# Optimization experiments

Measured on AMD Instinct MI355X. Metric: run time of the kernel, lower is better.

## Reference

```python
import jax, jax.numpy as jnp
import numpy as np

N_NODES = 10000
N_EDGES = 320000
F_NODE = 16
NUM_BESSEL = 8
M = 32           # env_embed_multiplicity
LAT = 128        # latent dimension
R_MAX = 5.0
P_CUT = 6.0      # polynomial cutoff order
AVG_NEIGH = 32.0
SQRT3 = 1.7320508075688772
SQRT2 = 1.4142135623730951


def _mlp(x, weights):
    # nequip ScalarMLPFunction: linear layers with 1/sqrt(fan_in) norm, silu between layers
    h = x
    n = len(weights)
    for i, W in enumerate(weights):
        h = h @ W * (1.0 / np.sqrt(W.shape[0]))
        if i < n - 1:
            h = jax.nn.silu(h)
    return h


def _weight_channels(Y, w):
    # MakeWeightedChannels: Y [E,4] = (0e | 1e), w [E,M,2] per-irrep weights -> [E,M,4]
    return jnp.concatenate([w[..., 0:1] * Y[:, None, 0:1],
                            w[..., 1:2] * Y[:, None, 1:4]], axis=-1)


def setup_inputs():
    key = jax.random.key(0)
    ks = jax.random.split(key, 16)

    def w(k, i, o):
        return jax.random.normal(k, (i, o), jnp.float32)

    two_body_in = 2 * F_NODE + NUM_BESSEL  # 40
    return {
        "coordinates": jax.random.uniform(ks[0], (N_NODES, 3), jnp.float32),
        "node_attrs": jax.random.uniform(ks[1], (N_NODES, F_NODE), jnp.float32),
        "edge_index": jax.random.randint(ks[2], (2, N_EDGES), 0, N_NODES),
        "W2b0": w(ks[3], two_body_in, 64),
        "W2b1": w(ks[4], 64, 128),
        "W2b2": w(ks[5], 128, LAT),
        "Wenv0": w(ks[6], LAT, 4 * M),       # initial-edge embed + env weights (2 irreps each)
        "Wlat0": w(ks[7], LAT + 2 * M, 128),
        "Wlat1": w(ks[8], 128, LAT),
        "Ws0": w(ks[9], 2 * M, M),            # e3nn Linear, scalar block (2 paths)
        "Wv0": w(ks[10], 3 * M, M),           # e3nn Linear, vector block (3 paths)
        "Wenv1": w(ks[11], LAT, 2 * M),
        "Wfin0": w(ks[12], LAT + 2 * M, 128),
        "Wfin1": w(ks[13], 128, LAT),
    }


def reference(coordinates, node_attrs, edge_index, W2b0, W2b1, W2b2, Wenv0,
              Wlat0, Wlat1, Ws0, Wv0, Wenv1, Wfin0, Wfin1):
    sender, center = edge_index[0], edge_index[1]
    vec = coordinates[center] - coordinates[sender]            # [E,3]
    r = jnp.sqrt(jnp.sum(vec * vec, axis=-1) + 1e-12)          # [E]
    u = r / R_MAX
    p = P_CUT
    fcut = (1.0 - (p + 1.0) * (p + 2.0) / 2.0 * u**p
            + p * (p + 2.0) * u**(p + 1.0)
            - p * (p + 1.0) / 2.0 * u**(p + 2.0))
    fcut = jnp.where(u < 1.0, fcut, 0.0)
    n = jnp.arange(1, NUM_BESSEL + 1, dtype=jnp.float32)
    bessel = np.sqrt(2.0 / R_MAX) * jnp.sin(n * jnp.pi * u[:, None]) / r[:, None]
    edge_feats = bessel * fcut[:, None]                        # [E,8]
    unit = vec / r[:, None]
    Y = jnp.concatenate([jnp.ones_like(r)[:, None], SQRT3 * unit], axis=-1)  # [E,4] component-normalized SH

    inv_sqrt_n = 1.0 / np.sqrt(AVG_NEIGH)
    E = r.shape[0]

    # two-body latent (layer 0)
    lat_in = jnp.concatenate([node_attrs[center], node_attrs[sender], edge_feats], -1)
    lat = _mlp(lat_in, (W2b0, W2b1, W2b2)) * fcut[:, None]     # [E,LAT]
    w_all = lat @ Wenv0 * (1.0 / np.sqrt(LAT))                 # [E,4M]
    w_edge = w_all[:, :2 * M].reshape(E, M, 2)
    w_env = w_all[:, 2 * M:].reshape(E, M, 2)
    feat = _weight_channels(Y, w_edge)                         # [E,M,4] initial edge embed
    env = jax.ops.segment_sum(_weight_channels(Y, w_env), center, num_segments=N_NODES)
    env = env[center] * inv_sqrt_n                             # [E,M,4]

    fs, fv = feat[..., 0], feat[..., 1:]
    es, ev = env[..., 0], env[..., 1:]
    # layer-0 tensor product instruction list (uuu, no weights)
    p0 = fs * es                               # 0e x 0e -> 0e
    p1 = jnp.sum(fv * ev, -1) / SQRT3          # 1e x 1e -> 0e
    p2 = fs[..., None] * ev                    # 0e x 1e -> 1e
    p3 = fv * es[..., None]                    # 1e x 0e -> 1e
    p4 = jnp.cross(fv, ev) / SQRT2             # 1e x 1e -> 1e
    scal0 = jnp.concatenate([p0, p1], -1)      # [E,2M] scalar outs (n_scalar_outs=2)
    # per-layer e3nn Linear
    s_mix = scal0 @ Ws0 * (1.0 / np.sqrt(2 * M))                         # [E,M]
    v_mix = jnp.einsum('eic,io->eoc', jnp.concatenate([p2, p3, p4], 1), Wv0) * (1.0 / np.sqrt(3 * M))  # [E,M,3]

    # latent resnet update (update param 0 -> sigmoid = 0.5)
    alpha = 0.5
    c_old = 1.0 / np.sqrt(alpha * alpha + 1.0)
    c_new = alpha * c_old
    new_lat = _mlp(jnp.concatenate([lat, scal0], -1), (Wlat0, Wlat1)) * fcut[:, None]
    lat = c_old * lat + c_new * new_lat

    # layer 1 env embedding + tensor product (last layer -> scalars only)
    w_env1 = (lat @ Wenv1 * (1.0 / np.sqrt(LAT))).reshape(E, M, 2)
    env1 = jax.ops.segment_sum(_weight_channels(Y, w_env1), center, num_segments=N_NODES)
    env1 = env1[center] * inv_sqrt_n
    q0 = s_mix * env1[..., 0]
    q1 = jnp.sum(v_mix * env1[..., 1:], -1) / SQRT3
    scal1 = jnp.concatenate([q0, q1], -1)      # [E,2M]

    new_lat = _mlp(jnp.concatenate([lat, scal1], -1), (Wfin0, Wfin1)) * fcut[:, None]
    lat = c_old * lat + c_new * new_lat

    node_out = jax.ops.segment_sum(lat, center, num_segments=N_NODES) * inv_sqrt_n
    return node_out
```

## Files before the change

kernel.cpp:

```cpp
#include <hip/hip_runtime.h>
#include <hip/hip_bf16.h>
#include <math.h>

typedef __hip_bfloat16 bf16;
typedef unsigned short us;
typedef __attribute__((ext_vector_type(8))) short short8;
typedef __attribute__((ext_vector_type(4))) float floatx4;

#define AMODE_PLAIN  0
#define AMODE_CONCAT 2
#define EPI_SPLIT    1
#define EPI_STORE    2
#define EPI_FCUT     3
#define EPI_RESID    4

#define INV_SQRT_N 0.17677669529663687f
#define INV_SQRT3  0.5773502691896258f
#define INV_SQRT2  0.7071067811865476f
#define C_OLD      0.8944271909999159f
#define C_NEW      0.4472135954999579f
#define PI_F       3.14159265358979323846f
#define SQRT3_F    1.7320508075688772f
#define BESSEL_PREF 0.6324555320336759f

__device__ __forceinline__ float b2f(bf16 x) { return __bfloat162float(x); }
__device__ __forceinline__ bf16  f2b(float x) { return __float2bfloat16(x); }
__device__ __forceinline__ us f2bu(float x) {
  bf16 h = f2b(x); us u; __builtin_memcpy(&u, &h, 2); return u;
}
__device__ __forceinline__ float silu_f(float v) { return v / (1.f + __expf(-v)); }
__device__ __forceinline__ floatx4 mfma16(short8 a, short8 b, floatx4 c) {
  return __builtin_amdgcn_mfma_f32_16x16x32_bf16(a, b, c, 0, 0, 0);
}
__device__ __forceinline__ short8 ld8(const void* p) {
  return *reinterpret_cast<const short8*>(p);
}

__global__ __launch_bounds__(256) void k_deg(
    const int* __restrict__ eidx, int E, int* __restrict__ deg) {
  int e = blockIdx.x * 256 + threadIdx.x;
  if (e < E) atomicAdd(&deg[eidx[E + e]], 1);
}

__global__ __launch_bounds__(1024) void k_scan(
    const int* __restrict__ deg, int N,
    int* __restrict__ rowptr, int* __restrict__ cursor) {
  __shared__ int part[1024];
  int t = threadIdx.x;
  int C = (N + 1023) / 1024;
  int base = t * C;
  int s = 0;
  for (int i = 0; i < C; ++i) { int idx = base + i; if (idx < N) s += deg[idx]; }
  part[t] = s;
  __syncthreads();
  for (int off = 1; off < 1024; off <<= 1) {
    int v = (t >= off) ? part[t - off] : 0;
    __syncthreads();
    part[t] += v;
    __syncthreads();
  }
  int excl = (t == 0) ? 0 : part[t - 1];
  for (int i = 0; i < C; ++i) {
    int idx = base + i;
    if (idx < N) { rowptr[idx] = excl; cursor[idx] = excl; excl += deg[idx]; }
  }
  if (t == 0) rowptr[N] = part[1023];
}

__global__ __launch_bounds__(256) void k_fill(
    const int* __restrict__ eidx, int E, int* __restrict__ cursor,
    int* __restrict__ eord, int* __restrict__ cent) {
  int e = blockIdx.x * 256 + threadIdx.x;
  if (e >= E) return;
  int c = eidx[E + e];
  int slot = atomicAdd(&cursor[c], 1);
  eord[slot] = e;
  cent[slot] = c;
}

__global__ __launch_bounds__(256) void k_geom(
    const float* __restrict__ coords, const float* __restrict__ nattr,
    const int* __restrict__ eidx, const int* __restrict__ eord, int E,
    float* __restrict__ fcut, float* __restrict__ Yb, bf16* __restrict__ a64) {
  int j = blockIdx.x * 256 + threadIdx.x;
  if (j >= E) return;
  int e = eord[j];
  int s = eidx[e], c = eidx[E + e];
  float dx = coords[c*3+0] - coords[s*3+0];
  float dy = coords[c*3+1] - coords[s*3+1];
  float dz = coords[c*3+2] - coords[s*3+2];
  float r = sqrtf(dx*dx + dy*dy + dz*dz + 1e-12f);
  float u = r * 0.2f;
  float u3 = u*u*u;
  float u6 = u3*u3, u7 = u6*u, u8 = u7*u;
  float fc = 1.f - 28.f*u6 + 48.f*u7 - 21.f*u8;
  fc = (u < 1.f) ? fc : 0.f;
  float inv_r = 1.f / r;
  fcut[j] = fc;
  Yb[j*4+0] = 1.f;
  Yb[j*4+1] = SQRT3_F * dx * inv_r;
  Yb[j*4+2] = SQRT3_F * dy * inv_r;
  Yb[j*4+3] = SQRT3_F * dz * inv_r;
  bf16* row = a64 + (long)j * 64;
  #pragma unroll
  for (int i = 0; i < 16; ++i) row[i]      = f2b(nattr[(long)c*16 + i]);
  #pragma unroll
  for (int i = 0; i < 16; ++i) row[16 + i] = f2b(nattr[(long)s*16 + i]);
  float pref = BESSEL_PREF * inv_r * fc;
  #pragma unroll
  for (int n = 1; n <= 8; ++n)
    row[32 + n - 1] = f2b(pref * sinf((float)n * PI_F * u));
  #pragma unroll
  for (int i = 40; i < 64; ++i) row[i] = f2b(0.f);
}

__device__ __forceinline__ void wp(const float* W, us* Wt, int K, int NOUT, int t) {
  int n = t / K, k = t % K;
  Wt[n * K + k] = f2bu(W[k * NOUT + n]);
}

__global__ __launch_bounds__(256) void k_wprep_all(
    const float* W2b0, const float* W2b1, const float* W2b2,
    const float* Wenv0, const float* Wlat0, const float* Wlat1,
    const float* Wenv1, const float* Wfin0, const float* Wfin1,
    const float* Ws0, const float* Wv0,
    us* W2b0p, us* W2b1t, us* W2b2t, us* Wenv0t, us* Wlat0t, us* Wlat1t,
    us* Wenv1t, us* Wfin0t, us* Wfin1t, us* Wmixt) {
  int t = blockIdx.x * 256 + threadIdx.x;
  if (t < 8192)  { wp(W2b1,  W2b1t,  64, 128, t); return; } t -= 8192;
  if (t < 16384) { wp(W2b2,  W2b2t, 128, 128, t); return; } t -= 16384;
  if (t < 16384) { wp(Wenv0, Wenv0t,128, 128, t); return; } t -= 16384;
  if (t < 24576) { wp(Wlat0, Wlat0t,192, 128, t); return; } t -= 24576;
  if (t < 16384) { wp(Wlat1, Wlat1t,128, 128, t); return; } t -= 16384;
  if (t < 8192)  { wp(Wenv1, Wenv1t,128,  64, t); return; } t -= 8192;
  if (t < 24576) { wp(Wfin0, Wfin0t,192, 128, t); return; } t -= 24576;
  if (t < 16384) { wp(Wfin1, Wfin1t,128, 128, t); return; } t -= 16384;
  if (t < 4096)  {
    int n = t >> 6, k = t & 63;
    W2b0p[n * 64 + k] = (k < 40) ? f2bu(W2b0[k * 64 + n]) : 0;
    return;
  } t -= 4096;
  if (t < 5120) {
    int o = t / 160, k = t % 160;
    float v = (k < 64) ? Ws0[k * 32 + o] : Wv0[(k - 64) * 32 + o];
    Wmixt[o * 160 + k] = f2bu(v);
  }
}

__global__ __launch_bounds__(256) void k_envg(
    const bf16* __restrict__ wenv, const float* __restrict__ Yb,
    const int* __restrict__ rowptr, int N, float* __restrict__ env) {
  int t = blockIdx.x * 256 + threadIdx.x;
  if (t >= N * 32) return;
  int n = t >> 5, m = t & 31;
  int j0 = rowptr[n], j1 = rowptr[n + 1];
  float a0 = 0.f, a1 = 0.f, a2 = 0.f, a3 = 0.f;
  for (int j = j0; j < j1; ++j) {
    float w0 = b2f(wenv[(long)j*64 + 2*m]);
    float w1 = b2f(wenv[(long)j*64 + 2*m + 1]);
    float4 y = *reinterpret_cast<const float4*>(&Yb[(long)j*4]);
    a0 += w0;
    a1 += w1 * y.y;
    a2 += w1 * y.z;
    a3 += w1 * y.w;
  }
  *reinterpret_cast<float4*>(&env[(long)n*128 + m*4]) = make_float4(a0, a1, a2, a3);
}

__global__ __launch_bounds__(256) void k_nodeg(
    const bf16* __restrict__ lat, const int* __restrict__ rowptr,
    int N, float* __restrict__ out) {
  int t = blockIdx.x * 256 + threadIdx.x;
  if (t >= N * 128) return;
  int n = t >> 7, j = t & 127;
  int j0 = rowptr[n], j1 = rowptr[n + 1];
  float s = 0.f;
  for (int q = j0; q < j1; ++q)
    s += b2f(lat[(long)q*128 + j]);
  out[t] = s * INV_SQRT_N;
}

template<int K, int NOUT, int EPI>
__global__ __launch_bounds__(256) void mgemm(
    const bf16* __restrict__ A, const us* __restrict__ Wt,
    bf16* __restrict__ out1, bf16* __restrict__ out2, float scale, int E) {
  constexpr int CT = NOUT / 64;
  int tid = threadIdx.x;
  int lane = tid & 63, w = tid >> 6;
  int nl = lane & 15, quad = lane >> 4;
  long e0 = (long)blockIdx.x * 64;

  floatx4 acc[4][CT];
  #pragma unroll
  for (int i = 0; i < 4; ++i)
    #pragma unroll
    for (int j = 0; j < CT; ++j) acc[i][j] = (floatx4){0.f,0.f,0.f,0.f};

  for (int k0 = 0; k0 < K; k0 += 32) {
    int kk = k0 + quad * 8;
    short8 af[4], bv[CT];
    #pragma unroll
    for (int et = 0; et < 4; ++et) {
      long eg = e0 + et*16 + nl;
      af[et] = (eg < E) ? ld8(A + eg * (long)K + kk) : (short8){0,0,0,0,0,0,0,0};
    }
    #pragma unroll
    for (int ct = 0; ct < CT; ++ct)
      bv[ct] = ld8(Wt + (long)(w*CT*16 + ct*16 + nl) * K + kk);
    #pragma unroll
    for (int et = 0; et < 4; ++et)
      #pragma unroll
      for (int ct = 0; ct < CT; ++ct)
        acc[et][ct] = mfma16(af[et], bv[ct], acc[et][ct]);
  }

  #pragma unroll
  for (int et = 0; et < 4; ++et)
    #pragma unroll
    for (int ct = 0; ct < CT; ++ct)
      #pragma unroll
      for (int r = 0; r < 4; ++r) {
        long eg = e0 + et*16 + quad*4 + r;
        if (eg >= E) continue;
        int col = w*CT*16 + ct*16 + nl;
        float v = acc[et][ct][r] * scale;
        if constexpr (EPI == EPI_SPLIT) {
          if (col < 64) out1[eg * 64 + col] = f2b(v);
          else          out2[eg * 64 + (col - 64)] = f2b(v);
        } else {
          out1[eg * NOUT + col] = f2b(v);
        }
      }
}

__global__ __launch_bounds__(256) void mfused3(
    const bf16* __restrict__ a64, const us* __restrict__ W0p,
    const us* __restrict__ W1t, const us* __restrict__ W2t,
    bf16* __restrict__ lat, const float* __restrict__ fcut,
    float s40, float s64, float s128, int E) {
  constexpr int H0P = 72, HP = 136;
  __shared__ __align__(16) us H0[64 * H0P];
  __shared__ __align__(16) us Hs[64 * HP];
  int tid = threadIdx.x;
  int lane = tid & 63, w = tid >> 6;
  int nl = lane & 15, quad = lane >> 4;
  long e0 = (long)blockIdx.x * 64;

  floatx4 a0[4];
  #pragma unroll
  for (int i = 0; i < 4; ++i) a0[i] = (floatx4){0.f,0.f,0.f,0.f};
  #pragma unroll
  for (int k0 = 0; k0 < 64; k0 += 32) {
    int kk = k0 + quad * 8;
    short8 af[4];
    #pragma unroll
    for (int et = 0; et < 4; ++et) {
      long eg = e0 + et*16 + nl;
      af[et] = (eg < E) ? ld8(a64 + eg * 64 + kk) : (short8){0,0,0,0,0,0,0,0};
    }
    short8 bv = ld8(W0p + (w*16 + nl) * 64 + kk);
    #pragma unroll
    for (int et = 0; et < 4; ++et) a0[et] = mfma16(af[et], bv, a0[et]);
  }
  #pragma unroll
  for (int et = 0; et < 4; ++et)
    #pragma unroll
    for (int r = 0; r < 4; ++r)
      H0[(et*16 + quad*4 + r) * H0P + w*16 + nl] = f2bu(silu_f(a0[et][r] * s40));
  __syncthreads();

  floatx4 acc[4][2];
  #pragma unroll
  for (int i = 0; i < 4; ++i)
    #pragma unroll
    for (int j = 0; j < 2; ++j) acc[i][j] = (floatx4){0.f,0.f,0.f,0.f};
  #pragma unroll
  for (int k0 = 0; k0 < 64; k0 += 32) {
    int kk = k0 + quad * 8;
    short8 af[4], bv[2];
    #pragma unroll
    for (int et = 0; et < 4; ++et)
      af[et] = ld8(&H0[(et*16 + nl) * H0P + kk]);
    #pragma unroll
    for (int ct = 0; ct < 2; ++ct)
      bv[ct] = ld8(W1t + (long)(w*32 + ct*16 + nl) * 64 + kk);
    #pragma unroll
    for (int et = 0; et < 4; ++et)
      #pragma unroll
      for (int ct = 0; ct < 2; ++ct)
        acc[et][ct] = mfma16(af[et], bv[ct], acc[et][ct]);
  }
  #pragma unroll
  for (int et = 0; et < 4; ++et)
    #pragma unroll
    for (int ct = 0; ct < 2; ++ct)
      #pragma unroll
      for (int r = 0; r < 4; ++r)
        Hs[(et*16 + quad*4 + r) * HP + w*32 + ct*16 + nl] =
            f2bu(silu_f(acc[et][ct][r] * s64));
  __syncthreads();

  #pragma unroll
  for (int i = 0; i < 4; ++i)
    #pragma unroll
    for (int j = 0; j < 2; ++j) acc[i][j] = (floatx4){0.f,0.f,0.f,0.f};
  #pragma unroll
  for (int k0 = 0; k0 < 128; k0 += 32) {
    int kk = k0 + quad * 8;
    short8 af[4], bv[2];
    #pragma unroll
    for (int et = 0; et < 4; ++et)
      af[et] = ld8(&Hs[(et*16 + nl) * HP + kk]);
    #pragma unroll
    for (int ct = 0; ct < 2; ++ct)
      bv[ct] = ld8(W2t + (long)(w*32 + ct*16 + nl) * 128 + kk);
    #pragma unroll
    for (int et = 0; et < 4; ++et)
      #pragma unroll
      for (int ct = 0; ct < 2; ++ct)
        acc[et][ct] = mfma16(af[et], bv[ct], acc[et][ct]);
  }
  #pragma unroll
  for (int et = 0; et < 4; ++et)
    #pragma unroll
    for (int ct = 0; ct < 2; ++ct)
      #pragma unroll
      for (int r = 0; r < 4; ++r) {
        long eg = e0 + et*16 + quad*4 + r;
        if (eg >= E) continue;
        lat[eg * 128 + w*32 + ct*16 + nl] =
            f2b(acc[et][ct][r] * s128 * fcut[eg]);
      }
}

template<int K, int AMODE, int EPI>
__global__ __launch_bounds__(256) void mfused(
    const bf16* __restrict__ A, const bf16* __restrict__ A2,
    const us* __restrict__ W0t, const us* __restrict__ W1t,
    bf16* __restrict__ outb, const float* __restrict__ fcut,
    float scale0, float scale1, int E) {
  constexpr int HP = 136;
  __shared__ __align__(16) us Hs[64 * HP];
  int tid = threadIdx.x;
  int lane = tid & 63, w = tid >> 6;
  int nl = lane & 15, quad = lane >> 4;
  long e0 = (long)blockIdx.x * 64;

  floatx4 acc[4][2];
  #pragma unroll
  for (int i = 0; i < 4; ++i)
    #pragma unroll
    for (int j = 0; j < 2; ++j) acc[i][j] = (floatx4){0.f,0.f,0.f,0.f};

  for (int k0 = 0; k0 < K; k0 += 32) {
    int kk = k0 + quad * 8;
    short8 af[4], bv[2];
    #pragma unroll
    for (int et = 0; et < 4; ++et) {
      long eg = e0 + et*16 + nl;
      if (eg < E) {
        const bf16* src;
        if constexpr (AMODE == AMODE_PLAIN) src = A + eg * (long)K + kk;
        else src = (k0 < 128) ? (A + eg * 128 + kk) : (A2 + eg * 64 + (kk - 128));
        af[et] = ld8(src);
      } else af[et] = (short8){0,0,0,0,0,0,0,0};
    }
    #pragma unroll
    for (int ct = 0; ct < 2; ++ct)
      bv[ct] = ld8(W0t + (long)(w*32 + ct*16 + nl) * K + kk);
    #pragma unroll
    for (int et = 0; et < 4; ++et)
      #pragma unroll
      for (int ct = 0; ct < 2; ++ct)
        acc[et][ct] = mfma16(af[et], bv[ct], acc[et][ct]);
  }

  #pragma unroll
  for (int et = 0; et < 4; ++et)
    #pragma unroll
    for (int ct = 0; ct < 2; ++ct)
      #pragma unroll
      for (int r = 0; r < 4; ++r)
        Hs[(et*16 + quad*4 + r) * HP + w*32 + ct*16 + nl] =
            f2bu(silu_f(acc[et][ct][r] * scale0));
  __syncthreads();

  #pragma unroll
  for (int i = 0; i < 4; ++i)
    #pragma unroll
    for (int j = 0; j < 2; ++j) acc[i][j] = (floatx4){0.f,0.f,0.f,0.f};

  #pragma unroll
  for (int k0 = 0; k0 < 128; k0 += 32) {
    int kk = k0 + quad * 8;
    short8 af[4], bv[2];
    #pragma unroll
    for (int et = 0; et < 4; ++et)
      af[et] = ld8(&Hs[(et*16 + nl) * HP + kk]);
    #pragma unroll
    for (int ct = 0; ct < 2; ++ct)
      bv[ct] = ld8(W1t + (long)(w*32 + ct*16 + nl) * 128 + kk);
    #pragma unroll
    for (int et = 0; et < 4; ++et)
      #pragma unroll
      for (int ct = 0; ct < 2; ++ct)
        acc[et][ct] = mfma16(af[et], bv[ct], acc[et][ct]);
  }

  #pragma unroll
  for (int et = 0; et < 4; ++et)
    #pragma unroll
    for (int ct = 0; ct < 2; ++ct)
      #pragma unroll
      for (int r = 0; r < 4; ++r) {
        long eg = e0 + et*16 + quad*4 + r;
        if (eg >= E) continue;
        int col = w*32 + ct*16 + nl;
        float fc = fcut[eg];
        float v = acc[et][ct][r] * scale1 * fc;
        if constexpr (EPI == EPI_FCUT) {
          outb[eg * 128 + col] = f2b(v);
        } else {
          long idx = eg * 128 + col;
          outb[idx] = f2b(C_OLD * b2f(outb[idx]) + C_NEW * v);
        }
      }
}

__global__ __launch_bounds__(256) void k_prod(
    const bf16* __restrict__ wedge, const float* __restrict__ env,
    const float* __restrict__ Yb, const int* __restrict__ cent, int E,
    bf16* __restrict__ scal) {
  long t = (long)blockIdx.x * 256 + threadIdx.x;
  if (t >= (long)E * 32) return;
  long e = t >> 5;
  int m = (int)(t & 31);
  int c = cent[e];
  float w0 = b2f(wedge[e*64 + 2*m]), w1 = b2f(wedge[e*64 + 2*m + 1]);
  const float* ep = env + (long)c*128 + m*4;
  float es  = ep[0] * INV_SQRT_N;
  float evx = ep[1] * INV_SQRT_N, evy = ep[2] * INV_SQRT_N, evz = ep[3] * INV_SQRT_N;
  float y1 = Yb[e*4+1], y2 = Yb[e*4+2], y3 = Yb[e*4+3];
  float fvx = w1*y1, fvy = w1*y2, fvz = w1*y3;
  scal[e*64 + m]      = f2b(w0 * es);
  scal[e*64 + 32 + m] = f2b((fvx*evx + fvy*evy + fvz*evz) * INV_SQRT3);
}

__global__ __launch_bounds__(256) void k_mix2(
    const bf16* __restrict__ wedge, const float* __restrict__ env,
    const float* __restrict__ env1, const float* __restrict__ Yb,
    const int* __restrict__ cent, const us* __restrict__ Wm,
    int E, bf16* __restrict__ scal) {
  constexpr int PP = 360;
  constexpr int RP = 132;
  __shared__ __align__(16) unsigned char SB[64 * PP * 2];
  __shared__ __align__(16) us Wl[32 * 160];
  us* P = (us*)SB;
  float* R = (float*)SB;
  int tid = threadIdx.x;
  int lane = tid & 63, w = tid >> 6;
  int nl = lane & 15, quad = lane >> 4;
  long e0 = (long)blockIdx.x * 64;

  for (int i = tid; i < 640; i += 256)
    *(short8*)&Wl[i * 8] = ld8(Wm + i * 8);

  int m = tid & 31;
  #pragma unroll
  for (int it = 0; it < 8; ++it) {
    int el = (tid >> 5) + it * 8;
    long e = e0 + el;
    if (e < E) {
      int c = cent[e];
      float w0 = b2f(wedge[e*64 + 2*m]), w1 = b2f(wedge[e*64 + 2*m + 1]);
      float4 ev4 = *(const float4*)(env + (long)c*128 + m*4);
      float4 y   = *(const float4*)(Yb + e*4);
      float es  = ev4.x * INV_SQRT_N;
      float evx = ev4.y * INV_SQRT_N, evy = ev4.z * INV_SQRT_N, evz = ev4.w * INV_SQRT_N;
      float fvx = w1*y.y, fvy = w1*y.z, fvz = w1*y.w;
      us* p = P + el * PP;
      p[m]       = f2bu(w0 * es);
      p[32 + m]  = f2bu((fvx*evx + fvy*evy + fvz*evz) * INV_SQRT3);
      p[64 + m]  = f2bu(w0 * evx);
      p[96 + m]  = f2bu(fvx * es);
      p[128 + m] = f2bu((fvy*evz - fvz*evy) * INV_SQRT2);
      p[160 + m] = f2bu(w0 * evy);
      p[192 + m] = f2bu(fvy * es);
      p[224 + m] = f2bu((fvz*evx - fvx*evz) * INV_SQRT2);
      p[256 + m] = f2bu(w0 * evz);
      p[288 + m] = f2bu(fvz * es);
      p[320 + m] = f2bu((fvx*evy - fvy*evx) * INV_SQRT2);
    } else {
      us* p = P + el * PP;
      #pragma unroll
      for (int q = 0; q < 11; ++q) p[q*32 + m] = 0;
    }
  }
  __syncthreads();

  floatx4 acc[4][2];
  #pragma unroll
  for (int i = 0; i < 4; ++i)
    #pragma unroll
    for (int j = 0; j < 2; ++j) acc[i][j] = (floatx4){0.f,0.f,0.f,0.f};
  int pbase  = (w == 0) ? 0 : 64 + (w - 1) * 96;
  int wkbase = (w == 0) ? 0 : 64;
  int ksteps = (w == 0) ? 2 : 3;
  for (int ks = 0; ks < ksteps; ++ks) {
    short8 af[4], bv[2];
    #pragma unroll
    for (int et = 0; et < 4; ++et)
      af[et] = ld8(&P[(et*16 + nl) * PP + pbase + ks*32 + quad*8]);
    #pragma unroll
    for (int ct = 0; ct < 2; ++ct)
      bv[ct] = ld8(&Wl[(ct*16 + nl) * 160 + wkbase + ks*32 + quad*8]);
    #pragma unroll
    for (int et = 0; et < 4; ++et)
      #pragma unroll
      for (int ct = 0; ct < 2; ++ct)
        acc[et][ct] = mfma16(af[et], bv[ct], acc[et][ct]);
  }
  __syncthreads();

  #pragma unroll
  for (int et = 0; et < 4; ++et)
    #pragma unroll
    for (int ct = 0; ct < 2; ++ct)
      #pragma unroll
      for (int r = 0; r < 4; ++r) {
        int el = et*16 + quad*4 + r;
        R[el * RP + w*32 + ct*16 + nl] = acc[et][ct][r];
      }
  __syncthreads();

  #pragma unroll
  for (int it = 0; it < 8; ++it) {
    int el = (tid >> 5) + it * 8;
    long e = e0 + el;
    if (e >= E) continue;
    int o = m;
    int c = cent[e];
    float4 e1 = *(const float4*)(env1 + (long)c*128 + o*4);
    float sr = R[el * RP + o];
    float vx = R[el * RP + 32 + o];
    float vy = R[el * RP + 64 + o];
    float vz = R[el * RP + 96 + o];
    float q0 = sr * 0.125f * (e1.x * INV_SQRT_N);
    float q1 = (vx*e1.y + vy*e1.z + vz*e1.w) *
               (0.10206207261596577f * INV_SQRT_N * INV_SQRT3);
    scal[e*64 + o]      = f2b(q0);
    scal[e*64 + 32 + o] = f2b(q1);
  }
}

extern "C" void kernel_launch(void* const* d_in, const int* in_sizes, int n_in,
                              void* d_out, int out_size, void* d_ws, size_t ws_size,
                              hipStream_t stream) {
  const float* coords = (const float*)d_in[0];
  const float* nattr  = (const float*)d_in[1];
  const int*   eidx   = (const int*)d_in[2];
  const float* W2b0   = (const float*)d_in[3];
  const float* W2b1   = (const float*)d_in[4];
  const float* W2b2   = (const float*)d_in[5];
  const float* Wenv0  = (const float*)d_in[6];
  const float* Wlat0  = (const float*)d_in[7];
  const float* Wlat1  = (const float*)d_in[8];
  const float* Ws0    = (const float*)d_in[9];
  const float* Wv0    = (const float*)d_in[10];
  const float* Wenv1  = (const float*)d_in[11];
  const float* Wfin0  = (const float*)d_in[12];
  const float* Wfin1  = (const float*)d_in[13];
  float* out = (float*)d_out;
  int E = in_sizes[2] / 2;
  int N = in_sizes[0] / 3;

  float* fcut   = (float*)d_ws;
  float* Yb     = fcut + (size_t)E;
  float* env    = Yb + (size_t)E*4;
  float* env1   = env + (size_t)N*128;
  int*   deg    = (int*)(env1 + (size_t)N*128);
  int*   rowptr = deg + N;
  int*   cursor = rowptr + (N + 8);
  int*   eord   = cursor + N;
  int*   cent   = eord + E;
  bf16*  b64    = (bf16*)(cent + E);
  bf16*  lat    = b64 + (size_t)E*64;
  bf16*  S      = lat + (size_t)E*128;
  us* W2b1t  = (us*)(S + (size_t)E*64);
  us* W2b2t  = W2b1t + 128*64;
  us* Wenv0t = W2b2t + 128*128;
  us* Wlat0t = Wenv0t + 128*128;
  us* Wlat1t = Wlat0t + 128*192;
  us* Wenv1t = Wlat1t + 128*128;
  us* Wfin0t = Wenv1t + 64*128;
  us* Wfin1t = Wfin0t + 128*192;
  us* W2b0p  = Wfin1t + 128*128;
  us* Wmixt  = W2b0p + 64*64;

  hipMemsetAsync(deg, 0, (size_t)N * sizeof(int), stream);

  dim3 blk(256);
  const float s40  = 0.15811388300841897f;
  const float s64  = 0.125f;
  const float s128 = 0.08838834764831845f;
  const float s192 = 0.07216878364870323f;
  int gB = (E + 63) / 64;
  int gE = (E + 255) / 256;

  k_deg<<<gE, blk, 0, stream>>>(eidx, E, deg);
  k_scan<<<1, 1024, 0, stream>>>(deg, N, rowptr, cursor);
  k_fill<<<gE, blk, 0, stream>>>(eidx, E, cursor, eord, cent);
  k_geom<<<gE, blk, 0, stream>>>(coords, nattr, eidx, eord, E, fcut, Yb, S );
  k_wprep_all<<<dim3(548), blk, 0, stream>>>(
      W2b0, W2b1, W2b2, Wenv0, Wlat0, Wlat1, Wenv1, Wfin0, Wfin1, Ws0, Wv0,
      W2b0p, W2b1t, W2b2t, Wenv0t, Wlat0t, Wlat1t, Wenv1t, Wfin0t, Wfin1t, Wmixt);

  mfused3<<<gB, blk, 0, stream>>>(
      S , W2b0p, W2b1t, W2b2t, lat, fcut, s40, s64, s128, E);

  mgemm<128,128,EPI_SPLIT><<<gB, blk, 0, stream>>>(
      lat, Wenv0t, b64, S , s128, E);

  k_envg<<<dim3((N*32 + 255) / 256), blk, 0, stream>>>(
      S , Yb, rowptr, N, env);

  k_prod<<<dim3((int)(((long)E*32 + 255) / 256)), blk, 0, stream>>>(
      b64, env, Yb, cent, E, S );

  mfused<192,AMODE_CONCAT,EPI_RESID><<<gB, blk, 0, stream>>>(
      lat, S , Wlat0t, Wlat1t, lat, fcut, s192, s128, E);

  mgemm<128,64,EPI_STORE><<<gB, blk, 0, stream>>>(
      lat, Wenv1t, S , nullptr, s128, E);

  k_envg<<<dim3((N*32 + 255) / 256), blk, 0, stream>>>(
      S , Yb, rowptr, N, env1);

  k_mix2<<<gB, blk, 0, stream>>>(
      b64, env, env1, Yb, cent, Wmixt, E, S );

  mfused<192,AMODE_CONCAT,EPI_RESID><<<gB, blk, 0, stream>>>(
      lat, S , Wfin0t, Wfin1t, lat, fcut, s192, s128, E);

  k_nodeg<<<dim3((N*128 + 255) / 256), blk, 0, stream>>>(
      lat, rowptr, N, out);
}
```

Before: 841.2 us.

## Stage activation tiles in LDS and preload weight fragments into registers

```diff
diff --git a/kernel.cpp b/kernel.cpp
--- a/kernel.cpp
+++ b/kernel.cpp
@@ -11,7 +11,6 @@
 #define AMODE_CONCAT 2
 #define EPI_SPLIT    1
 #define EPI_STORE    2
-#define EPI_FCUT     3
 #define EPI_RESID    4
 
 #define INV_SQRT_N 0.17677669529663687f
@@ -35,6 +34,7 @@
 __device__ __forceinline__ short8 ld8(const void* p) {
   return *reinterpret_cast<const short8*>(p);
 }
+#define ZERO8 ((short8){0,0,0,0,0,0,0,0})
 
 __global__ __launch_bounds__(256) void k_deg(
     const int* __restrict__ eidx, int E, int* __restrict__ deg) {
@@ -180,38 +180,51 @@
   out[t] = s * INV_SQRT_N;
 }
 
-template<int K, int NOUT, int EPI>
+template<int NOUT, int EPI>
 __global__ __launch_bounds__(256) void mgemm(
     const bf16* __restrict__ A, const us* __restrict__ Wt,
     bf16* __restrict__ out1, bf16* __restrict__ out2, float scale, int E) {
+  constexpr int K = 128, KP = 136, NC = 4;
   constexpr int CT = NOUT / 64;
+  __shared__ __align__(16) us As[64 * KP];
   int tid = threadIdx.x;
   int lane = tid & 63, w = tid >> 6;
   int nl = lane & 15, quad = lane >> 4;
   long e0 = (long)blockIdx.x * 64;
 
+  short8 wf[NC][CT];
+  #pragma unroll
+  for (int kc = 0; kc < NC; ++kc)
+    #pragma unroll
+    for (int ct = 0; ct < CT; ++ct)
+      wf[kc][ct] = ld8(Wt + (long)(w*CT*16 + ct*16 + nl) * K + kc*32 + quad*8);
+
+  #pragma unroll
+  for (int it = 0; it < 4; ++it) {
+    int i = tid + it * 256;
+    int row = i >> 4, col = (i & 15) * 8;
+    long eg = e0 + row;
+    short8 v = (eg < E) ? ld8(A + eg * 128 + col) : ZERO8;
+    *(short8*)&As[row * KP + col] = v;
+  }
+  __syncthreads();
+
   floatx4 acc[4][CT];
   #pragma unroll
   for (int i = 0; i < 4; ++i)
     #pragma unroll
     for (int j = 0; j < CT; ++j) acc[i][j] = (floatx4){0.f,0.f,0.f,0.f};
-
-  for (int k0 = 0; k0 < K; k0 += 32) {
-    int kk = k0 + quad * 8;
-    short8 af[4], bv[CT];
-    #pragma unroll
-    for (int et = 0; et < 4; ++et) {
-      long eg = e0 + et*16 + nl;
-      af[et] = (eg < E) ? ld8(A + eg * (long)K + kk) : (short8){0,0,0,0,0,0,0,0};
-    }
-    #pragma unroll
-    for (int ct = 0; ct < CT; ++ct)
-      bv[ct] = ld8(Wt + (long)(w*CT*16 + ct*16 + nl) * K + kk);
+  #pragma unroll
+  for (int kc = 0; kc < NC; ++kc) {
+    short8 af[4];
+    #pragma unroll
+    for (int et = 0; et < 4; ++et)
+      af[et] = ld8(&As[(et*16 + nl) * KP + kc*32 + quad*8]);
     #pragma unroll
     for (int et = 0; et < 4; ++et)
       #pragma unroll
       for (int ct = 0; ct < CT; ++ct)
-        acc[et][ct] = mfma16(af[et], bv[ct], acc[et][ct]);
+        acc[et][ct] = mfma16(af[et], wf[kc][ct], acc[et][ct]);
   }
 
   #pragma unroll
@@ -237,36 +250,58 @@
     const bf16* __restrict__ a64, const us* __restrict__ W0p,
     const us* __restrict__ W1t, const us* __restrict__ W2t,
     bf16* __restrict__ lat, const float* __restrict__ fcut,
-    float s40, float s64, float s128, int E) {
-  constexpr int H0P = 72, HP = 136;
-  __shared__ __align__(16) us H0[64 * H0P];
+    float s40, float s64s, float s128, int E) {
+  constexpr int AP = 72, HP = 136;
+  __shared__ __align__(16) us As[64 * AP];
+  __shared__ __align__(16) us H0[64 * AP];
   __shared__ __align__(16) us Hs[64 * HP];
   int tid = threadIdx.x;
   int lane = tid & 63, w = tid >> 6;
   int nl = lane & 15, quad = lane >> 4;
   long e0 = (long)blockIdx.x * 64;
 
+  short8 w0f[2], w1f[2][2], w2f[4][2];
+  #pragma unroll
+  for (int kc = 0; kc < 2; ++kc)
+    w0f[kc] = ld8(W0p + (w*16 + nl) * 64 + kc*32 + quad*8);
+  #pragma unroll
+  for (int kc = 0; kc < 2; ++kc)
+    #pragma unroll
+    for (int ct = 0; ct < 2; ++ct)
+      w1f[kc][ct] = ld8(W1t + (long)(w*32 + ct*16 + nl) * 64 + kc*32 + quad*8);
+  #pragma unroll
+  for (int kc = 0; kc < 4; ++kc)
+    #pragma unroll
+    for (int ct = 0; ct < 2; ++ct)
+      w2f[kc][ct] = ld8(W2t + (long)(w*32 + ct*16 + nl) * 128 + kc*32 + quad*8);
+
+  #pragma unroll
+  for (int it = 0; it < 2; ++it) {
+    int i = tid + it * 256;
+    int row = i >> 3, col = (i & 7) * 8;
+    long eg = e0 + row;
+    short8 v = (eg < E) ? ld8(a64 + eg * 64 + col) : ZERO8;
+    *(short8*)&As[row * AP + col] = v;
+  }
+  __syncthreads();
+
   floatx4 a0[4];
   #pragma unroll
   for (int i = 0; i < 4; ++i) a0[i] = (floatx4){0.f,0.f,0.f,0.f};
   #pragma unroll
-  for (int k0 = 0; k0 < 64; k0 += 32) {
-    int kk = k0 + quad * 8;
+  for (int kc = 0; kc < 2; ++kc) {
     short8 af[4];
     #pragma unroll
-    for (int et = 0; et < 4; ++et) {
-      long eg = e0 + et*16 + nl;
-      af[et] = (eg < E) ? ld8(a64 + eg * 64 + kk) : (short8){0,0,0,0,0,0,0,0};
-    }
-    short8 bv = ld8(W0p + (w*16 + nl) * 64 + kk);
-    #pragma unroll
-    for (int et = 0; et < 4; ++et) a0[et] = mfma16(af[et], bv, a0[et]);
+    for (int et = 0; et < 4; ++et)
+      af[et] = ld8(&As[(et*16 + nl) * AP + kc*32 + quad*8]);
+    #pragma unroll
+    for (int et = 0; et < 4; ++et) a0[et] = mfma16(af[et], w0f[kc], a0[et]);
   }
   #pragma unroll
   for (int et = 0; et < 4; ++et)
     #pragma unroll
     for (int r = 0; r < 4; ++r)
-      H0[(et*16 + quad*4 + r) * H0P + w*16 + nl] = f2bu(silu_f(a0[et][r] * s40));
+      H0[(et*16 + quad*4 + r) * AP + w*16 + nl] = f2bu(silu_f(a0[et][r] * s40));
   __syncthreads();
 
   floatx4 acc[4][2];
@@ -275,20 +310,16 @@
     #pragma unroll
     for (int j = 0; j < 2; ++j) acc[i][j] = (floatx4){0.f,0.f,0.f,0.f};
   #pragma unroll
-  for (int k0 = 0; k0 < 64; k0 += 32) {
-    int kk = k0 + quad * 8;
-    short8 af[4], bv[2];
-    #pragma unroll
-    for (int et = 0; et < 4; ++et)
-      af[et] = ld8(&H0[(et*16 + nl) * H0P + kk]);
-    #pragma unroll
-    for (int ct = 0; ct < 2; ++ct)
-      bv[ct] = ld8(W1t + (long)(w*32 + ct*16 + nl) * 64 + kk);
+  for (int kc = 0; kc < 2; ++kc) {
+    short8 af[4];
+    #pragma unroll
+    for (int et = 0; et < 4; ++et)
+      af[et] = ld8(&H0[(et*16 + nl) * AP + kc*32 + quad*8]);
     #pragma unroll
     for (int et = 0; et < 4; ++et)
       #pragma unroll
       for (int ct = 0; ct < 2; ++ct)
-        acc[et][ct] = mfma16(af[et], bv[ct], acc[et][ct]);
+        acc[et][ct] = mfma16(af[et], w1f[kc][ct], acc[et][ct]);
   }
   #pragma unroll
   for (int et = 0; et < 4; ++et)
@@ -297,7 +328,7 @@
       #pragma unroll
       for (int r = 0; r < 4; ++r)
         Hs[(et*16 + quad*4 + r) * HP + w*32 + ct*16 + nl] =
-            f2bu(silu_f(acc[et][ct][r] * s64));
+            f2bu(silu_f(acc[et][ct][r] * s64s));
   __syncthreads();
 
   #pragma unroll
@@ -305,20 +336,16 @@
     #pragma unroll
     for (int j = 0; j < 2; ++j) acc[i][j] = (floatx4){0.f,0.f,0.f,0.f};
   #pragma unroll
-  for (int k0 = 0; k0 < 128; k0 += 32) {
-    int kk = k0 + quad * 8;
-    short8 af[4], bv[2];
-    #pragma unroll
-    for (int et = 0; et < 4; ++et)
-      af[et] = ld8(&Hs[(et*16 + nl) * HP + kk]);
-    #pragma unroll
-    for (int ct = 0; ct < 2; ++ct)
-      bv[ct] = ld8(W2t + (long)(w*32 + ct*16 + nl) * 128 + kk);
+  for (int kc = 0; kc < 4; ++kc) {
+    short8 af[4];
+    #pragma unroll
+    for (int et = 0; et < 4; ++et)
+      af[et] = ld8(&Hs[(et*16 + nl) * HP + kc*32 + quad*8]);
     #pragma unroll
     for (int et = 0; et < 4; ++et)
       #pragma unroll
       for (int ct = 0; ct < 2; ++ct)
-        acc[et][ct] = mfma16(af[et], bv[ct], acc[et][ct]);
+        acc[et][ct] = mfma16(af[et], w2f[kc][ct], acc[et][ct]);
   }
   #pragma unroll
   for (int et = 0; et < 4; ++et)
@@ -333,47 +360,69 @@
       }
 }
 
-template<int K, int AMODE, int EPI>
+template<int EPI>
 __global__ __launch_bounds__(256) void mfused(
     const bf16* __restrict__ A, const bf16* __restrict__ A2,
     const us* __restrict__ W0t, const us* __restrict__ W1t,
     bf16* __restrict__ outb, const float* __restrict__ fcut,
     float scale0, float scale1, int E) {
-  constexpr int HP = 136;
+  constexpr int K = 192, KP = 200, NC0 = 6, HP = 136;
+  __shared__ __align__(16) us As[64 * KP];
   __shared__ __align__(16) us Hs[64 * HP];
   int tid = threadIdx.x;
   int lane = tid & 63, w = tid >> 6;
   int nl = lane & 15, quad = lane >> 4;
   long e0 = (long)blockIdx.x * 64;
 
+  short8 w0f[NC0][2];
+  #pragma unroll
+  for (int kc = 0; kc < NC0; ++kc)
+    #pragma unroll
+    for (int ct = 0; ct < 2; ++ct)
+      w0f[kc][ct] = ld8(W0t + (long)(w*32 + ct*16 + nl) * K + kc*32 + quad*8);
+
+  #pragma unroll
+  for (int it = 0; it < 4; ++it) {
+    int i = tid + it * 256;
+    int row = i >> 4, col = (i & 15) * 8;
+    long eg = e0 + row;
+    short8 v = (eg < E) ? ld8(A + eg * 128 + col) : ZERO8;
+    *(short8*)&As[row * KP + col] = v;
+  }
+  #pragma unroll
+  for (int it = 0; it < 2; ++it) {
+    int i = tid + it * 256;
+    int row = i >> 3, col = (i & 7) * 8;
+    long eg = e0 + row;
+    short8 v = (eg < E) ? ld8(A2 + eg * 64 + col) : ZERO8;
+    *(short8*)&As[row * KP + 128 + col] = v;
+  }
+  __syncthreads();
+
   floatx4 acc[4][2];
   #pragma unroll
   for (int i = 0; i < 4; ++i)
     #pragma unroll
     for (int j = 0; j < 2; ++j) acc[i][j] = (floatx4){0.f,0.f,0.f,0.f};
-
-  for (int k0 = 0; k0 < K; k0 += 32) {
-    int kk = k0 + quad * 8;
-    short8 af[4], bv[2];
-    #pragma unroll
-    for (int et = 0; et < 4; ++et) {
-      long eg = e0 + et*16 + nl;
-      if (eg < E) {
-        const bf16* src;
-        if constexpr (AMODE == AMODE_PLAIN) src = A + eg * (long)K + kk;
-        else src = (k0 < 128) ? (A + eg * 128 + kk) : (A2 + eg * 64 + (kk - 128));
-        af[et] = ld8(src);
-      } else af[et] = (short8){0,0,0,0,0,0,0,0};
-    }
-    #pragma unroll
-    for (int ct = 0; ct < 2; ++ct)
-      bv[ct] = ld8(W0t + (long)(w*32 + ct*16 + nl) * K + kk);
+  #pragma unroll
+  for (int kc = 0; kc < NC0; ++kc) {
+    short8 af[4];
+    #pragma unroll
+    for (int et = 0; et < 4; ++et)
+      af[et] = ld8(&As[(et*16 + nl) * KP + kc*32 + quad*8]);
     #pragma unroll
     for (int et = 0; et < 4; ++et)
       #pragma unroll
       for (int ct = 0; ct < 2; ++ct)
-        acc[et][ct] = mfma16(af[et], bv[ct], acc[et][ct]);
-  }
+        acc[et][ct] = mfma16(af[et], w0f[kc][ct], acc[et][ct]);
+  }
+
+  short8 w1f[4][2];
+  #pragma unroll
+  for (int kc = 0; kc < 4; ++kc)
+    #pragma unroll
+    for (int ct = 0; ct < 2; ++ct)
+      w1f[kc][ct] = ld8(W1t + (long)(w*32 + ct*16 + nl) * 128 + kc*32 + quad*8);
 
   #pragma unroll
   for (int et = 0; et < 4; ++et)
@@ -389,22 +438,17 @@
   for (int i = 0; i < 4; ++i)
     #pragma unroll
     for (int j = 0; j < 2; ++j) acc[i][j] = (floatx4){0.f,0.f,0.f,0.f};
-
-  #pragma unroll
-  for (int k0 = 0; k0 < 128; k0 += 32) {
-    int kk = k0 + quad * 8;
-    short8 af[4], bv[2];
-    #pragma unroll
-    for (int et = 0; et < 4; ++et)
-      af[et] = ld8(&Hs[(et*16 + nl) * HP + kk]);
-    #pragma unroll
-    for (int ct = 0; ct < 2; ++ct)
-      bv[ct] = ld8(W1t + (long)(w*32 + ct*16 + nl) * 128 + kk);
+  #pragma unroll
+  for (int kc = 0; kc < 4; ++kc) {
+    short8 af[4];
+    #pragma unroll
+    for (int et = 0; et < 4; ++et)
+      af[et] = ld8(&Hs[(et*16 + nl) * HP + kc*32 + quad*8]);
     #pragma unroll
     for (int et = 0; et < 4; ++et)
       #pragma unroll
       for (int ct = 0; ct < 2; ++ct)
-        acc[et][ct] = mfma16(af[et], bv[ct], acc[et][ct]);
+        acc[et][ct] = mfma16(af[et], w1f[kc][ct], acc[et][ct]);
   }
 
   #pragma unroll
@@ -416,14 +460,9 @@
         long eg = e0 + et*16 + quad*4 + r;
         if (eg >= E) continue;
         int col = w*32 + ct*16 + nl;
-        float fc = fcut[eg];
-        float v = acc[et][ct][r] * scale1 * fc;
-        if constexpr (EPI == EPI_FCUT) {
-          outb[eg * 128 + col] = f2b(v);
-        } else {
-          long idx = eg * 128 + col;
-          outb[idx] = f2b(C_OLD * b2f(outb[idx]) + C_NEW * v);
-        }
+        float v = acc[et][ct][r] * scale1 * fcut[eg];
+        long idx = eg * 128 + col;
+        outb[idx] = f2b(C_OLD * b2f(outb[idx]) + C_NEW * v);
       }
 }
 
@@ -618,7 +657,7 @@
   mfused3<<<gB, blk, 0, stream>>>(
       S , W2b0p, W2b1t, W2b2t, lat, fcut, s40, s64, s128, E);
 
-  mgemm<128,128,EPI_SPLIT><<<gB, blk, 0, stream>>>(
+  mgemm<128,EPI_SPLIT><<<gB, blk, 0, stream>>>(
       lat, Wenv0t, b64, S , s128, E);
 
   k_envg<<<dim3((N*32 + 255) / 256), blk, 0, stream>>>(
@@ -627,10 +666,10 @@
   k_prod<<<dim3((int)(((long)E*32 + 255) / 256)), blk, 0, stream>>>(
       b64, env, Yb, cent, E, S );
 
-  mfused<192,AMODE_CONCAT,EPI_RESID><<<gB, blk, 0, stream>>>(
+  mfused<EPI_RESID><<<gB, blk, 0, stream>>>(
       lat, S , Wlat0t, Wlat1t, lat, fcut, s192, s128, E);
 
-  mgemm<128,64,EPI_STORE><<<gB, blk, 0, stream>>>(
+  mgemm<64,EPI_STORE><<<gB, blk, 0, stream>>>(
       lat, Wenv1t, S , nullptr, s128, E);
 
   k_envg<<<dim3((N*32 + 255) / 256), blk, 0, stream>>>(
@@ -639,7 +678,7 @@
   k_mix2<<<gB, blk, 0, stream>>>(
       b64, env, env1, Yb, cent, Wmixt, E, S );
 
-  mfused<192,AMODE_CONCAT,EPI_RESID><<<gB, blk, 0, stream>>>(
+  mfused<EPI_RESID><<<gB, blk, 0, stream>>>(
       lat, S , Wfin0t, Wfin1t, lat, fcut, s192, s128, E);
 
   k_nodeg<<<dim3((N*128 + 255) / 256), blk, 0, stream>>>(
```

Measured after the change: 766.1 us. -8.9%, faster.
